# Optimization experiments

Hardware: AMD Instinct MI355X
Metric: run time of the kernel (lower is better)

The kernel has to match this reference:

```python
import jax, jax.numpy as jnp
import numpy as np


def setup_inputs() -> dict:
    key = jax.random.key(0)
    # (B, C, H, W) with H == W, required by the original module's broadcasting.
    x = jax.random.normal(key, (16, 64, 256, 256), dtype=jnp.float32)
    return {"x": x}


def reference(x):
    """Naive real DFT of the original module, computed as a separable contraction.

    Original math (after resolving the meshgrid 'xy' indexing, H == W == N):
      real[b,c,u,v] = sum_{i,j} x[b,c,i,j] * cos(2*pi*(j*u + i*v)/N)
      imag[b,c,u,v] = sum_{i,j} x[b,c,i,j] * sin(-2*pi*(j*u + i*v)/N)
    with u in [0, N/2), v in [0, N/2).
    We use cos(a+b)=cos a cos b - sin a sin b to factorize into matmuls,
    avoiding the (B,C,N,N,N/2,N/2) broadcast intermediate.
    """
    B, C, H, W = x.shape
    assert H == W, "original module's broadcasting requires square input"
    N = H
    K = N // 2
    two_pi = jnp.asarray(2.0 * np.pi, dtype=x.dtype)
    n = jnp.arange(N, dtype=x.dtype) / N          # spatial index / N
    k = jnp.arange(K, dtype=x.dtype)              # frequency index
    ang = two_pi * n[:, None] * k[None, :]        # (N, K)
    Cm = jnp.cos(ang)                             # (N, K)
    Sm = jnp.sin(ang)                             # (N, K)

    # Contract W-axis j against frequency u, then H-axis i against frequency v.
    A = jnp.einsum('bcij,ju->bciu', x, Cm)        # sum_j x * cos(2pi j u / N)
    Bt = jnp.einsum('bcij,ju->bciu', x, Sm)       # sum_j x * sin(2pi j u / N)
    real = jnp.einsum('bciu,iv->bcuv', A, Cm) - jnp.einsum('bciu,iv->bcuv', Bt, Sm)
    imag = -(jnp.einsum('bciu,iv->bcuv', Bt, Cm) + jnp.einsum('bciu,iv->bcuv', A, Sm))
    return real, imag
```

## Files before the change

### kernel.cpp

```cpp
#include <hip/hip_runtime.h>
#include <hip/hip_bf16.h>


typedef __attribute__((ext_vector_type(8))) short short8;
typedef __attribute__((ext_vector_type(4))) short bf16x4;
typedef __attribute__((ext_vector_type(4))) float f32x4;
typedef __attribute__((ext_vector_type(2))) float f32x2;

typedef union { short8 s8; unsigned u[4]; } pk8;
typedef union { bf16x4 s4; unsigned u[2]; } pk4;

#define NN 256
#define KF 128
#define NIMG 1024

__device__ __align__(16) short g_Ct[KF * NN];
__device__ __align__(16) short g_Stn[KF * NN];
__device__ __align__(16) short g_T2cE[64 * 128];
__device__ __align__(16) short g_T2cO[64 * 128];
__device__ __align__(16) short g_T2sE[64 * 128];
__device__ __align__(16) short g_T2sO[64 * 128];

__device__ __forceinline__ short f2bf(float f) {
    union { float f; unsigned u; } v; v.f = f;
    unsigned r = v.u + 0x7FFFu + ((v.u >> 16) & 1u);
    return (short)(r >> 16);
}

__device__ __forceinline__ unsigned cvtpk(float lo, float hi) {
    unsigned r;
    asm("v_cvt_pk_bf16_f32 %0, %1, %2" : "=v"(r) : "v"(lo), "v"(hi));
    return r;
}

__global__ void gen_tables() {
    int tid = blockIdx.x * blockDim.x + threadIdx.x;
    const float w = 0.02454369260617026f;
    if (tid < KF * NN) {
        int u = tid >> 8;
        int j = tid & 255;
        int phase = (u * j) & 255;
        float s, c;
        sincosf((float)phase * w, &s, &c);
        g_Ct[tid]  = f2bf(c);
        g_Stn[tid] = f2bf(-s);
    }
    if (tid < 64 * 128) {
        int s = tid >> 7;
        int i = tid & 127;
        int pe = (i * (2 * s)) & 255;
        int po = (i * (2 * s + 1)) & 255;
        float se, ce, so, co;
        sincosf((float)pe * w, &se, &ce);
        sincosf((float)po * w, &so, &co);
        g_T2cE[tid] = f2bf(ce);
        g_T2cO[tid] = f2bf(co);
        g_T2sE[tid] = f2bf(se);
        g_T2sO[tid] = f2bf(so);
    }
}

#define MFMA(a, b, c) __builtin_amdgcn_mfma_f32_16x16x32_bf16(a, b, c, 0, 0, 0)

__global__ __launch_bounds__(512, 4) void freq_dft(const float* __restrict__ x,
                                                   float* __restrict__ out) {
    __shared__ __align__(16) char lds[65536];

    const int bid = blockIdx.x;
    const int cc  = bid & 7;
    const int q   = bid >> 3;
    const int h   = q & 1;
    const int img = cc + ((q >> 1) << 3);

    const float* __restrict__ X = x + (size_t)img * (NN * NN);
    float* __restrict__ outR = out + (size_t)img * (KF * KF);
    float* __restrict__ outI = outR + (size_t)NIMG * (KF * KF);

    const int lane = threadIdx.x & 63;
    const int wave = threadIdx.x >> 6;
    const int l15  = lane & 15;
    const int lk8  = (lane >> 4) << 3;
    const int lr4  = (lane >> 4) << 2;
    const int wst  = wave;

    {
        const short* __restrict__ srcC = g_Ct  + h * 64 * NN;
        const short* __restrict__ srcS = g_Stn + h * 64 * NN;
        #pragma unroll
        for (int k = 0; k < 4; ++k) {
            int slot = threadIdx.x + k * 512;
            int row  = slot >> 5;
            int chk  = slot & 31;
            int byte = row * 512 + ((chk << 4) ^ ((row & 7) << 4));
            short8 vC = *(const short8*)(srcC + row * NN + chk * 8);
            short8 vS = *(const short8*)(srcS + row * NN + chk * 8);
            *(short8*)(lds + byte)         = vC;
            *(short8*)(lds + 32768 + byte) = vS;
        }
    }
    __syncthreads();

    f32x4 accA[2][4], accB[2][4];
    {
        const int i0 = wave * 16;
        #pragma unroll
        for (int fi = 0; fi < 2; ++fi)
            #pragma unroll
            for (int fu = 0; fu < 4; ++fu) {
                accA[fi][fu] = (f32x4){0.f, 0.f, 0.f, 0.f};
                accB[fi][fu] = (f32x4){0.f, 0.f, 0.f, 0.f};
            }
        const float* __restrict__ xp0 = X + (i0 + l15) * NN + lk8;
        const float* __restrict__ xp1 = X + (i0 + 128 + l15) * NN + lk8;
        const int jA = (wst & 7) * 32;
        const int jB = ((wst + 1) & 7) * 32;
        f32x4 a0 = *(const f32x4*)(xp0 + jA), a1 = *(const f32x4*)(xp0 + jA + 4);
        f32x4 a2 = *(const f32x4*)(xp1 + jA), a3 = *(const f32x4*)(xp1 + jA + 4);
        f32x4 b0 = *(const f32x4*)(xp0 + jB), b1 = *(const f32x4*)(xp0 + jB + 4);
        f32x4 b2 = *(const f32x4*)(xp1 + jB), b3 = *(const f32x4*)(xp1 + jB + 4);
        #pragma unroll
        for (int t = 0; t < 8; ++t) {
            const int j0 = ((t + wst) & 7) * 32;
            f32x4 c0 = a0, c1 = a1, c2 = a2, c3 = a3;
            a0 = b0; a1 = b1; a2 = b2; a3 = b3;
            if (t < 6) {
                const int jn = ((t + 2 + wst) & 7) * 32;
                b0 = *(const f32x4*)(xp0 + jn); b1 = *(const f32x4*)(xp0 + jn + 4);
                b2 = *(const f32x4*)(xp1 + jn); b3 = *(const f32x4*)(xp1 + jn + 4);
            }
            pk8 x0u, x1u;
            x0u.u[0] = cvtpk(c0[0], c0[1]); x0u.u[1] = cvtpk(c0[2], c0[3]);
            x0u.u[2] = cvtpk(c1[0], c1[1]); x0u.u[3] = cvtpk(c1[2], c1[3]);
            x1u.u[0] = cvtpk(c2[0], c2[1]); x1u.u[1] = cvtpk(c2[2], c2[3]);
            x1u.u[2] = cvtpk(c3[0], c3[1]); x1u.u[3] = cvtpk(c3[2], c3[3]);
            short8 xb0 = x0u.s8;
            short8 xb1 = x1u.s8;
            short8 ca[4], sa[4];
            #pragma unroll
            for (int fu = 0; fu < 4; ++fu) {
                int row  = fu * 16 + l15;
                int byte = row * 512 + (((j0 + lk8) * 2) ^ ((row & 7) << 4));
                ca[fu] = *(const short8*)(lds + byte);
                sa[fu] = *(const short8*)(lds + 32768 + byte);
            }
            #pragma unroll
            for (int fu = 0; fu < 4; ++fu) {
                accA[0][fu] = MFMA(xb0, ca[fu], accA[0][fu]);
                accA[1][fu] = MFMA(xb1, ca[fu], accA[1][fu]);
                accB[0][fu] = MFMA(xb0, sa[fu], accB[0][fu]);
                accB[1][fu] = MFMA(xb1, sa[fu], accB[1][fu]);
            }
        }
    }
    __syncthreads();

    {
        const int kb = wave * 16 + lr4;
        #pragma unroll
        for (int fu = 0; fu < 4; ++fu) {
            f32x4 eA = accA[0][fu] + accA[1][fu];
            f32x4 oA = accA[0][fu] - accA[1][fu];
            f32x4 eB = accB[0][fu] + accB[1][fu];
            f32x4 oB = accB[0][fu] - accB[1][fu];
            int ul  = fu * 16 + l15;
            int sw  = (ul & 7) << 4;
            int byE = ul * 512 + ((kb * 2) ^ sw);
            int byO = ul * 512 + (((kb + 128) * 2) ^ sw);
            pk4 ea, oa, eb, ob;
            ea.u[0] = cvtpk(eA[0], eA[1]); ea.u[1] = cvtpk(eA[2], eA[3]);
            oa.u[0] = cvtpk(oA[0], oA[1]); oa.u[1] = cvtpk(oA[2], oA[3]);
            eb.u[0] = cvtpk(eB[0], eB[1]); eb.u[1] = cvtpk(eB[2], eB[3]);
            ob.u[0] = cvtpk(oB[0], oB[1]); ob.u[1] = cvtpk(oB[2], oB[3]);
            *(bf16x4*)(lds + byE)         = ea.s4;
            *(bf16x4*)(lds + byO)         = oa.s4;
            *(bf16x4*)(lds + 32768 + byE) = eb.s4;
            *(bf16x4*)(lds + 32768 + byO) = ob.s4;
        }
    }
    __syncthreads();

    {
        const int wu = wave >> 2;
        const int vt = wave & 3;
        const short8 smask = {(short)0x8000, (short)0x8000, (short)0x8000, (short)0x8000,
                              (short)0x8000, (short)0x8000, (short)0x8000, (short)0x8000};
        f32x4 accRE[2], accRO[2], accIE[2], accIO[2];
        #pragma unroll
        for (int fu = 0; fu < 2; ++fu) {
            accRE[fu] = (f32x4){0.f, 0.f, 0.f, 0.f};
            accRO[fu] = (f32x4){0.f, 0.f, 0.f, 0.f};
            accIE[fu] = (f32x4){0.f, 0.f, 0.f, 0.f};
            accIO[fu] = (f32x4){0.f, 0.f, 0.f, 0.f};
        }
        const short* __restrict__ pcE = g_T2cE + (vt * 16 + l15) * 128 + lk8;
        const short* __restrict__ pcO = g_T2cO + (vt * 16 + l15) * 128 + lk8;
        const short* __restrict__ psE = g_T2sE + (vt * 16 + l15) * 128 + lk8;
        const short* __restrict__ psO = g_T2sO + (vt * 16 + l15) * 128 + lk8;
        const int iA = (wst & 3) * 32;
        const int iB = ((wst + 1) & 3) * 32;
        short8 AcE = *(const short8*)(pcE + iA), AcO = *(const short8*)(pcO + iA);
        short8 AsE = *(const short8*)(psE + iA), AsO = *(const short8*)(psO + iA);
        short8 BcE = *(const short8*)(pcE + iB), BcO = *(const short8*)(pcO + iB);
        short8 BsE = *(const short8*)(psE + iB), BsO = *(const short8*)(psO + iB);
        #pragma unroll
        for (int t = 0; t < 4; ++t) {
            const int is = ((t + wst) & 3) * 32;
            short8 cE = AcE, cO = AcO, sE = AsE, sO = AsO;
            AcE = BcE; AcO = BcO; AsE = BsE; AsO = BsO;
            if (t < 2) {
                const int in = ((t + 2 + wst) & 3) * 32;
                BcE = *(const short8*)(pcE + in); BcO = *(const short8*)(pcO + in);
                BsE = *(const short8*)(psE + in); BsO = *(const short8*)(psO + in);
            }
            short8 sEn = sE ^ smask;
            short8 sOn = sO ^ smask;
            short8 eA[2], oA[2], eB[2], oB[2];
            #pragma unroll
            for (int fu = 0; fu < 2; ++fu) {
                int ul  = wu * 32 + fu * 16 + l15;
                int sw  = (ul & 7) << 4;
                int byE = ul * 512 + (((is + lk8) * 2) ^ sw);
                int byO = ul * 512 + (((is + 128 + lk8) * 2) ^ sw);
                eA[fu] = *(const short8*)(lds + byE);
                oA[fu] = *(const short8*)(lds + byO);
                eB[fu] = *(const short8*)(lds + 32768 + byE);
                oB[fu] = *(const short8*)(lds + 32768 + byO);
            }
            accRE[0] = MFMA(eA[0], cE, accRE[0]); accRE[1] = MFMA(eA[1], cE, accRE[1]);
            accRO[0] = MFMA(oA[0], cO, accRO[0]); accRO[1] = MFMA(oA[1], cO, accRO[1]);
            accIE[0] = MFMA(eB[0], cE, accIE[0]); accIE[1] = MFMA(eB[1], cE, accIE[1]);
            accIO[0] = MFMA(oB[0], cO, accIO[0]); accIO[1] = MFMA(oB[1], cO, accIO[1]);
            accRE[0] = MFMA(eB[0], sE, accRE[0]); accRE[1] = MFMA(eB[1], sE, accRE[1]);
            accRO[0] = MFMA(oB[0], sO, accRO[0]); accRO[1] = MFMA(oB[1], sO, accRO[1]);
            accIE[0] = MFMA(eA[0], sEn, accIE[0]); accIE[1] = MFMA(eA[1], sEn, accIE[1]);
            accIO[0] = MFMA(oA[0], sOn, accIO[0]); accIO[1] = MFMA(oA[1], sOn, accIO[1]);
        }
        #pragma unroll
        for (int fu = 0; fu < 2; ++fu)
            #pragma unroll
            for (int r = 0; r < 4; ++r) {
                int u = h * 64 + wu * 32 + fu * 16 + lr4 + r;
                int v = vt * 32 + 2 * l15;
                f32x2 vr = {accRE[fu][r], accRO[fu][r]};
                f32x2 vi = {accIE[fu][r], accIO[fu][r]};
                *(f32x2*)(outR + u * KF + v) = vr;
                *(f32x2*)(outI + u * KF + v) = vi;
            }
    }
}

extern "C" void kernel_launch(void* const* d_in, const int* in_sizes, int n_in,
                              void* d_out, int out_size, void* d_ws, size_t ws_size,
                              hipStream_t stream) {
    const float* x = (const float*)d_in[0];
    float* out = (float*)d_out;
    gen_tables<<<dim3((KF * NN + 255) / 256), dim3(256), 0, stream>>>();
    freq_dft<<<dim3(NIMG * 2), dim3(512), 0, stream>>>(x, out);
}
```

Baseline: 134.5 us.

## Fold first-stage DFT along W using even/odd frequency symmetry

The first-stage contraction over the W axis is split into even and odd output frequencies. Input columns j and j+128 are pre-combined as sums and differences, which halves the K dimension of the MFMA work and the size of the cos/sin tables staged in LDS. The big Ct/Stn tables are dropped; the smaller even/odd tables are reused, with the sine sign flipped on load. The table generator becomes smaller, and the LDS write layout of intermediates is remapped to interleave even and odd rows. This adds fp32 add/sub work before the bf16 conversion and changes index mapping, which could introduce subtle errors.

```diff
diff --git a/kernel.cpp b/kernel.cpp
--- a/kernel.cpp
+++ b/kernel.cpp
@@ -14,12 +14,10 @@
 #define KF 128
 #define NIMG 1024
 
-__device__ __align__(16) short g_Ct[KF * NN];
-__device__ __align__(16) short g_Stn[KF * NN];
-__device__ __align__(16) short g_T2cE[64 * 128];
-__device__ __align__(16) short g_T2cO[64 * 128];
-__device__ __align__(16) short g_T2sE[64 * 128];
-__device__ __align__(16) short g_T2sO[64 * 128];
+__device__ __align__(16) short gcE[64 * 128];
+__device__ __align__(16) short gcO[64 * 128];
+__device__ __align__(16) short gsE[64 * 128];
+__device__ __align__(16) short gsO[64 * 128];
 
 __device__ __forceinline__ short f2bf(float f) {
     union { float f; unsigned u; } v; v.f = f;
@@ -35,29 +33,19 @@
 
 __global__ void gen_tables() {
     int tid = blockIdx.x * blockDim.x + threadIdx.x;
+    if (tid >= 64 * 128) return;
     const float w = 0.02454369260617026f;
-    if (tid < KF * NN) {
-        int u = tid >> 8;
-        int j = tid & 255;
-        int phase = (u * j) & 255;
-        float s, c;
-        sincosf((float)phase * w, &s, &c);
-        g_Ct[tid]  = f2bf(c);
-        g_Stn[tid] = f2bf(-s);
-    }
-    if (tid < 64 * 128) {
-        int s = tid >> 7;
-        int i = tid & 127;
-        int pe = (i * (2 * s)) & 255;
-        int po = (i * (2 * s + 1)) & 255;
-        float se, ce, so, co;
-        sincosf((float)pe * w, &se, &ce);
-        sincosf((float)po * w, &so, &co);
-        g_T2cE[tid] = f2bf(ce);
-        g_T2cO[tid] = f2bf(co);
-        g_T2sE[tid] = f2bf(se);
-        g_T2sO[tid] = f2bf(so);
-    }
+    int m = tid >> 7;
+    int j = tid & 127;
+    int pe = (j * (2 * m)) & 255;
+    int po = (j * (2 * m + 1)) & 255;
+    float se, ce, so, co;
+    sincosf((float)pe * w, &se, &ce);
+    sincosf((float)po * w, &so, &co);
+    gcE[tid] = f2bf(ce);
+    gcO[tid] = f2bf(co);
+    gsE[tid] = f2bf(se);
+    gsO[tid] = f2bf(so);
 }
 
 #define MFMA(a, b, c) __builtin_amdgcn_mfma_f32_16x16x32_bf16(a, b, c, 0, 0, 0)
@@ -83,19 +71,28 @@
     const int lr4  = (lane >> 4) << 2;
     const int wst  = wave;
 
-    {
-        const short* __restrict__ srcC = g_Ct  + h * 64 * NN;
-        const short* __restrict__ srcS = g_Stn + h * 64 * NN;
-        #pragma unroll
-        for (int k = 0; k < 4; ++k) {
-            int slot = threadIdx.x + k * 512;
-            int row  = slot >> 5;
-            int chk  = slot & 31;
-            int byte = row * 512 + ((chk << 4) ^ ((row & 7) << 4));
-            short8 vC = *(const short8*)(srcC + row * NN + chk * 8);
-            short8 vS = *(const short8*)(srcS + row * NN + chk * 8);
-            *(short8*)(lds + byte)         = vC;
-            *(short8*)(lds + 32768 + byte) = vS;
+    const short8 smask = {(short)0x8000, (short)0x8000, (short)0x8000, (short)0x8000,
+                          (short)0x8000, (short)0x8000, (short)0x8000, (short)0x8000};
+
+    {
+        #pragma unroll
+        for (int k = 0; k < 2; ++k) {
+            int c   = threadIdx.x + k * 512;
+            int row = c >> 4, chk = c & 15;
+            int byte = row * 256 + ((chk << 4) ^ ((row & 7) << 4));
+            const short* src = (row < 32 ? gcE + (h * 32 + row) * 128
+                                         : gcO + (h * 32 + row - 32) * 128) + chk * 8;
+            *(short8*)(lds + byte) = *(const short8*)src;
+        }
+        #pragma unroll
+        for (int k = 0; k < 2; ++k) {
+            int c   = threadIdx.x + k * 512;
+            int row = c >> 4, chk = c & 15;
+            int byte = row * 256 + ((chk << 4) ^ ((row & 7) << 4));
+            const short* src = (row < 32 ? gsE + (h * 32 + row) * 128
+                                         : gsO + (h * 32 + row - 32) * 128) + chk * 8;
+            short8 v = *(const short8*)src;
+            *(short8*)(lds + 16384 + byte) = v ^ smask;
         }
     }
     __syncthreads();
@@ -110,46 +107,82 @@
                 accA[fi][fu] = (f32x4){0.f, 0.f, 0.f, 0.f};
                 accB[fi][fu] = (f32x4){0.f, 0.f, 0.f, 0.f};
             }
-        const float* __restrict__ xp0 = X + (i0 + l15) * NN + lk8;
-        const float* __restrict__ xp1 = X + (i0 + 128 + l15) * NN + lk8;
-        const int jA = (wst & 7) * 32;
-        const int jB = ((wst + 1) & 7) * 32;
-        f32x4 a0 = *(const f32x4*)(xp0 + jA), a1 = *(const f32x4*)(xp0 + jA + 4);
-        f32x4 a2 = *(const f32x4*)(xp1 + jA), a3 = *(const f32x4*)(xp1 + jA + 4);
-        f32x4 b0 = *(const f32x4*)(xp0 + jB), b1 = *(const f32x4*)(xp0 + jB + 4);
-        f32x4 b2 = *(const f32x4*)(xp1 + jB), b3 = *(const f32x4*)(xp1 + jB + 4);
-        #pragma unroll
-        for (int t = 0; t < 8; ++t) {
-            const int j0 = ((t + wst) & 7) * 32;
-            f32x4 c0 = a0, c1 = a1, c2 = a2, c3 = a3;
-            a0 = b0; a1 = b1; a2 = b2; a3 = b3;
-            if (t < 6) {
-                const int jn = ((t + 2 + wst) & 7) * 32;
-                b0 = *(const f32x4*)(xp0 + jn); b1 = *(const f32x4*)(xp0 + jn + 4);
-                b2 = *(const f32x4*)(xp1 + jn); b3 = *(const f32x4*)(xp1 + jn + 4);
-            }
-            pk8 x0u, x1u;
-            x0u.u[0] = cvtpk(c0[0], c0[1]); x0u.u[1] = cvtpk(c0[2], c0[3]);
-            x0u.u[2] = cvtpk(c1[0], c1[1]); x0u.u[3] = cvtpk(c1[2], c1[3]);
-            x1u.u[0] = cvtpk(c2[0], c2[1]); x1u.u[1] = cvtpk(c2[2], c2[3]);
-            x1u.u[2] = cvtpk(c3[0], c3[1]); x1u.u[3] = cvtpk(c3[2], c3[3]);
-            short8 xb0 = x0u.s8;
-            short8 xb1 = x1u.s8;
-            short8 ca[4], sa[4];
-            #pragma unroll
-            for (int fu = 0; fu < 4; ++fu) {
-                int row  = fu * 16 + l15;
-                int byte = row * 512 + (((j0 + lk8) * 2) ^ ((row & 7) << 4));
-                ca[fu] = *(const short8*)(lds + byte);
-                sa[fu] = *(const short8*)(lds + 32768 + byte);
-            }
-            #pragma unroll
-            for (int fu = 0; fu < 4; ++fu) {
-                accA[0][fu] = MFMA(xb0, ca[fu], accA[0][fu]);
-                accA[1][fu] = MFMA(xb1, ca[fu], accA[1][fu]);
-                accB[0][fu] = MFMA(xb0, sa[fu], accB[0][fu]);
-                accB[1][fu] = MFMA(xb1, sa[fu], accB[1][fu]);
-            }
+        const float* __restrict__ xL = X + (i0 + l15) * NN + lk8;
+        const float* __restrict__ xH = X + (i0 + 128 + l15) * NN + lk8;
+        const int jP = (wst & 3) * 32;
+        f32x4 r0 = *(const f32x4*)(xL + jP),       r1 = *(const f32x4*)(xL + jP + 4);
+        f32x4 r2 = *(const f32x4*)(xL + jP + 128), r3 = *(const f32x4*)(xL + jP + 132);
+        f32x4 r4 = *(const f32x4*)(xH + jP),       r5 = *(const f32x4*)(xH + jP + 4);
+        f32x4 r6 = *(const f32x4*)(xH + jP + 128), r7 = *(const f32x4*)(xH + jP + 132);
+        #pragma unroll
+        for (int t = 0; t < 4; ++t) {
+            const int j0 = ((t + wst) & 3) * 32;
+            pk8 xeL, xoL, xeH, xoH;
+            {
+                f32x4 e = r0 + r2, o = r0 - r2;
+                xeL.u[0] = cvtpk(e[0], e[1]); xeL.u[1] = cvtpk(e[2], e[3]);
+                xoL.u[0] = cvtpk(o[0], o[1]); xoL.u[1] = cvtpk(o[2], o[3]);
+            }
+            {
+                f32x4 e = r1 + r3, o = r1 - r3;
+                xeL.u[2] = cvtpk(e[0], e[1]); xeL.u[3] = cvtpk(e[2], e[3]);
+                xoL.u[2] = cvtpk(o[0], o[1]); xoL.u[3] = cvtpk(o[2], o[3]);
+            }
+            {
+                f32x4 e = r4 + r6, o = r4 - r6;
+                xeH.u[0] = cvtpk(e[0], e[1]); xeH.u[1] = cvtpk(e[2], e[3]);
+                xoH.u[0] = cvtpk(o[0], o[1]); xoH.u[1] = cvtpk(o[2], o[3]);
+            }
+            {
+                f32x4 e = r5 + r7, o = r5 - r7;
+                xeH.u[2] = cvtpk(e[0], e[1]); xeH.u[3] = cvtpk(e[2], e[3]);
+                xoH.u[2] = cvtpk(o[0], o[1]); xoH.u[3] = cvtpk(o[2], o[3]);
+            }
+            short8 XE0 = xeL.s8, XO0 = xoL.s8, XE1 = xeH.s8, XO1 = xoH.s8;
+            if (t < 3) {
+                const int jn = ((t + 1 + wst) & 3) * 32;
+                r0 = *(const f32x4*)(xL + jn);       r1 = *(const f32x4*)(xL + jn + 4);
+                r2 = *(const f32x4*)(xL + jn + 128); r3 = *(const f32x4*)(xL + jn + 132);
+            }
+            short8 ca0, ca1, sa0, sa1;
+            {
+                int row = l15;
+                int byte = row * 256 + (((j0 + lk8) * 2) ^ ((row & 7) << 4));
+                ca0 = *(const short8*)(lds + byte);
+                sa0 = *(const short8*)(lds + 16384 + byte);
+            }
+            {
+                int row = 16 + l15;
+                int byte = row * 256 + (((j0 + lk8) * 2) ^ ((row & 7) << 4));
+                ca1 = *(const short8*)(lds + byte);
+                sa1 = *(const short8*)(lds + 16384 + byte);
+            }
+            accA[0][0] = MFMA(XE0, ca0, accA[0][0]); accA[1][0] = MFMA(XE1, ca0, accA[1][0]);
+            accB[0][0] = MFMA(XE0, sa0, accB[0][0]); accB[1][0] = MFMA(XE1, sa0, accB[1][0]);
+            accA[0][1] = MFMA(XE0, ca1, accA[0][1]); accA[1][1] = MFMA(XE1, ca1, accA[1][1]);
+            accB[0][1] = MFMA(XE0, sa1, accB[0][1]); accB[1][1] = MFMA(XE1, sa1, accB[1][1]);
+            if (t < 3) {
+                const int jn = ((t + 1 + wst) & 3) * 32;
+                r4 = *(const f32x4*)(xH + jn);       r5 = *(const f32x4*)(xH + jn + 4);
+                r6 = *(const f32x4*)(xH + jn + 128); r7 = *(const f32x4*)(xH + jn + 132);
+            }
+            short8 ca2, ca3, sa2, sa3;
+            {
+                int row = 32 + l15;
+                int byte = row * 256 + (((j0 + lk8) * 2) ^ ((row & 7) << 4));
+                ca2 = *(const short8*)(lds + byte);
+                sa2 = *(const short8*)(lds + 16384 + byte);
+            }
+            {
+                int row = 48 + l15;
+                int byte = row * 256 + (((j0 + lk8) * 2) ^ ((row & 7) << 4));
+                ca3 = *(const short8*)(lds + byte);
+                sa3 = *(const short8*)(lds + 16384 + byte);
+            }
+            accA[0][2] = MFMA(XO0, ca2, accA[0][2]); accA[1][2] = MFMA(XO1, ca2, accA[1][2]);
+            accB[0][2] = MFMA(XO0, sa2, accB[0][2]); accB[1][2] = MFMA(XO1, sa2, accB[1][2]);
+            accA[0][3] = MFMA(XO0, ca3, accA[0][3]); accA[1][3] = MFMA(XO1, ca3, accA[1][3]);
+            accB[0][3] = MFMA(XO0, sa3, accB[0][3]); accB[1][3] = MFMA(XO1, sa3, accB[1][3]);
         }
     }
     __syncthreads();
@@ -162,7 +195,7 @@
             f32x4 oA = accA[0][fu] - accA[1][fu];
             f32x4 eB = accB[0][fu] + accB[1][fu];
             f32x4 oB = accB[0][fu] - accB[1][fu];
-            int ul  = fu * 16 + l15;
+            int ul  = 2 * ((fu & 1) * 16 + l15) + (fu >> 1);
             int sw  = (ul & 7) << 4;
             int byE = ul * 512 + ((kb * 2) ^ sw);
             int byO = ul * 512 + (((kb + 128) * 2) ^ sw);
@@ -182,8 +215,6 @@
     {
         const int wu = wave >> 2;
         const int vt = wave & 3;
-        const short8 smask = {(short)0x8000, (short)0x8000, (short)0x8000, (short)0x8000,
-                              (short)0x8000, (short)0x8000, (short)0x8000, (short)0x8000};
         f32x4 accRE[2], accRO[2], accIE[2], accIO[2];
         #pragma unroll
         for (int fu = 0; fu < 2; ++fu) {
@@ -192,10 +223,10 @@
             accIE[fu] = (f32x4){0.f, 0.f, 0.f, 0.f};
             accIO[fu] = (f32x4){0.f, 0.f, 0.f, 0.f};
         }
-        const short* __restrict__ pcE = g_T2cE + (vt * 16 + l15) * 128 + lk8;
-        const short* __restrict__ pcO = g_T2cO + (vt * 16 + l15) * 128 + lk8;
-        const short* __restrict__ psE = g_T2sE + (vt * 16 + l15) * 128 + lk8;
-        const short* __restrict__ psO = g_T2sO + (vt * 16 + l15) * 128 + lk8;
+        const short* __restrict__ pcE = gcE + (vt * 16 + l15) * 128 + lk8;
+        const short* __restrict__ pcO = gcO + (vt * 16 + l15) * 128 + lk8;
+        const short* __restrict__ psE = gsE + (vt * 16 + l15) * 128 + lk8;
+        const short* __restrict__ psO = gsO + (vt * 16 + l15) * 128 + lk8;
         const int iA = (wst & 3) * 32;
         const int iB = ((wst + 1) & 3) * 32;
         short8 AcE = *(const short8*)(pcE + iA), AcO = *(const short8*)(pcO + iA);
@@ -254,6 +285,6 @@
                               hipStream_t stream) {
     const float* x = (const float*)d_in[0];
     float* out = (float*)d_out;
-    gen_tables<<<dim3((KF * NN + 255) / 256), dim3(256), 0, stream>>>();
+    gen_tables<<<dim3(32), dim3(256), 0, stream>>>();
     freq_dft<<<dim3(NIMG * 2), dim3(512), 0, stream>>>(x, out);
 }
```

Result: no change. 134.0 us (median of 2 runs) (-0.3%).
